# Performance work log

Hardware: AMD Instinct MI355X
Metric: run time of the kernel (lower is better)

Reference implementation:

```python
import jax, jax.numpy as jnp
import numpy as np

N, T, E, H, K = 16, 1024, 1024, 256, 3
MAX_OUT = 4 * T          # static upper bound on upsampled length (padded; torch uses dynamic max)
DUR_FACTOR = 1.0
MIN_DUR = 0
LN_EPS = 1e-5


def setup_inputs() -> dict:
    key = jax.random.key(0)
    ks = jax.random.split(key, 6)
    seqs = jax.random.normal(ks[0], (N, T, E), dtype=jnp.float32)
    lens = jax.random.randint(ks[1], (N,), T // 2, T + 1)
    padding_mask = jnp.arange(T)[None, :] < lens[:, None]  # True = valid frame
    s = 0.02
    return {
        "seqs": seqs,
        "conv1_w": jax.random.normal(ks[2], (H, E, K), jnp.float32) * s,
        "conv1_b": jnp.zeros((H,), jnp.float32),
        "ln1_g": jnp.ones((H,), jnp.float32),
        "ln1_b": jnp.zeros((H,), jnp.float32),
        "conv2_w": jax.random.normal(ks[3], (H, H, K), jnp.float32) * s,
        "conv2_b": jnp.zeros((H,), jnp.float32),
        "ln2_g": jnp.ones((H,), jnp.float32),
        "ln2_b": jnp.zeros((H,), jnp.float32),
        "proj_w": jax.random.normal(ks[4], (H,), jnp.float32) * s,
        "proj_b": jnp.float32(1.1),  # pushes mean duration to ~2 frames
        "padding_mask": padding_mask,
    }


def _conv1d(x, w, b):
    # x: [N, C_in, T], w: [C_out, C_in, K], 'same' padding for K=3
    y = jax.lax.conv_general_dilated(x, w, window_strides=(1,), padding=[(1, 1)],
                                     dimension_numbers=("NCH", "OIH", "NCH"))
    return y + b[None, :, None]


def _layernorm(x, g, b):
    mu = jnp.mean(x, axis=-1, keepdims=True)
    var = jnp.mean(jnp.square(x - mu), axis=-1, keepdims=True)
    return (x - mu) * jax.lax.rsqrt(var + LN_EPS) * g + b


def _variance_predictor(seqs, padding_mask, c1w, c1b, g1, b1, c2w, c2b, g2, b2, pw, pb):
    m = padding_mask[..., None].astype(seqs.dtype)  # [N, T, 1]
    x = seqs * m
    x = jax.nn.relu(_conv1d(x.transpose(0, 2, 1), c1w, c1b)).transpose(0, 2, 1)  # [N, T, H]
    x = _layernorm(x, g1, b1)
    # dropout in eval mode = identity
    x = x * m
    x = jax.nn.relu(_conv1d(x.transpose(0, 2, 1), c2w, c2b)).transpose(0, 2, 1)
    x = _layernorm(x, g2, b2)
    return jnp.einsum("nth,h->nt", x, pw) + pb  # log durations [N, T]


def reference(seqs, conv1_w, conv1_b, ln1_g, ln1_b, conv2_w, conv2_b, ln2_g, ln2_b,
              proj_w, proj_b, padding_mask):
    log_dur = _variance_predictor(seqs, padding_mask, conv1_w, conv1_b, ln1_g, ln1_b,
                                  conv2_w, conv2_b, ln2_g, ln2_b, proj_w, proj_b)
    dur = jnp.round((jnp.exp(log_dur) - 1.0) * DUR_FACTOR).astype(jnp.int32)
    dur = jnp.maximum(dur, MIN_DUR)
    dur = jnp.where(padding_mask, dur, 0)  # apply_padding_mask on integer durations

    # HardUpsampling: output position t takes source frame i = searchsorted(cumsum(dur), t, 'right')
    cum = jnp.cumsum(dur, axis=1)                 # [N, T]
    seq_lens = cum[:, -1]                         # [N]
    pos = jnp.arange(MAX_OUT, dtype=jnp.int32)    # [MAX_OUT]
    idx = jax.vmap(lambda c: jnp.searchsorted(c, pos, side="right"))(cum)  # [N, MAX_OUT]
    idx = jnp.clip(idx, 0, T - 1)
    up = jnp.take_along_axis(seqs, idx[:, :, None], axis=1)  # [N, MAX_OUT, E]
    valid = pos[None, :] < seq_lens[:, None]
    up = jnp.where(valid[:, :, None], up, 0.0)
    return up, seq_lens
```

## Files before the change

### kernel.cpp

```cpp
#include <hip/hip_runtime.h>

#define N_ 16
#define T_ 1024
#define E_ 1024
#define H_ 256
#define MAXOUT 4096
#define M_ (N_ * T_)
#define NJ 768
#define NJ16 48

typedef _Float16 half_t;
typedef __attribute__((ext_vector_type(8))) _Float16 f16x8;
typedef __attribute__((ext_vector_type(4))) _Float16 f16x4;
typedef __attribute__((ext_vector_type(4))) float f32x4;

constexpr size_t Y1_OFF  = 0;
constexpr size_t Y2_OFF  = 25165824;
constexpr size_t A0P_OFF = 50331648;
constexpr size_t A2P_OFF = 83886080;

constexpr size_t B1P_OFF  = 0;
constexpr size_t B2P_OFF  = 1572864;
constexpr size_t DUR_OFF  = 1966080;
constexpr size_t CUM_OFF  = 2031616;

__device__ __forceinline__ float mask_at(const unsigned char* __restrict__ raw, int i) {
    if (raw[1] == 1) return raw[i] ? 1.0f : 0.0f;
    return reinterpret_cast<const int*>(raw)[i] ? 1.0f : 0.0f;
}

__device__ __forceinline__ void gload_lds16(const void* g, void* l) {
    __builtin_amdgcn_global_load_lds(
        (const __attribute__((address_space(1))) unsigned int*)g,
        (__attribute__((address_space(3))) unsigned int*)l, 16, 0, 0);
}

__global__ __launch_bounds__(256) void prep_all_kernel(
    const float* __restrict__ X, const unsigned char* __restrict__ mraw,
    const float* __restrict__ w1, const float* __restrict__ w2,
    half_t* __restrict__ A0p, half_t* __restrict__ B1p, half_t* __restrict__ B2p) {
    const int bid = blockIdx.x;
    if (bid < 1024) {
        const int bm = bid;
        const int l = threadIdx.x & 63;
        const int bk4 = threadIdx.x >> 6;
        const int row = bm * 16 + (l & 15);
        const float mv = mask_at(mraw, row);
        const float* src = X + (size_t)row * E_ + ((l >> 4) * 8);
#pragma unroll
        for (int g = 0; g < 8; ++g) {
            const int bk = g * 4 + bk4;
            float4 v0 = *reinterpret_cast<const float4*>(src + bk * 32);
            float4 v1 = *reinterpret_cast<const float4*>(src + bk * 32 + 4);
            float v[8] = {v0.x, v0.y, v0.z, v0.w, v1.x, v1.y, v1.z, v1.w};
            f16x8 h8;
#pragma unroll
            for (int j = 0; j < 8; ++j) h8[j] = (half_t)(v[j] * mv);
            *reinterpret_cast<f16x8*>(A0p + ((size_t)(bm * 32 + bk) * 64 + l) * 8) = h8;
        }
    } else {
        const bool isW1 = (bid < 1024 + 384);
        const int c = (isW1 ? (bid - 1024) : (bid - 1408)) * 256 + threadIdx.x;
        const int EIN = isW1 ? E_ : H_;
        const float* w = isW1 ? w1 : w2;
        half_t* Bp = isW1 ? B1p : B2p;
        const int l = c & 63;
        const int t = c >> 6;
        const int bj = t % NJ16;
        const int bk = t / NJ16;
        const int j = bj * 16 + (l & 15);
        const int k = j >> 8;
        const int h = j & 255;
        const int e0 = bk * 32 + ((l >> 4) * 8);
        f16x8 h8;
#pragma unroll
        for (int jj = 0; jj < 8; ++jj)
            h8[jj] = (half_t)w[((size_t)h * EIN + e0 + jj) * 3 + k];
        *reinterpret_cast<f16x8*>(Bp + (size_t)c * 8) = h8;
    }
}

template <int NBK>
__global__ __launch_bounds__(256, 4) void gemm_f16_kernel(
    const half_t* __restrict__ Ap, const half_t* __restrict__ Bp,
    half_t* __restrict__ Y) {
    __shared__ __align__(16) half_t lds[2][2][4096];
    const int tid = threadIdx.x;
    const int l = tid & 63;
    const int wv = tid >> 6;
    const int wr = wv >> 1, wc = wv & 1;
    const int bm0 = blockIdx.x * 8;
    const int bj0 = blockIdx.y * 8;

    f32x4 acc[4][4] = {};

    auto stage = [&](int kb, int buf) {
#pragma unroll
        for (int s = 0; s < 2; ++s) {
            const int q = tid + 256 * s;
            const int blk = q >> 6;
            const int ql = q & 63;
            gload_lds16(Ap + (((size_t)(bm0 + blk) * NBK + kb) * 64 + ql) * 8,
                        &lds[buf][0][(size_t)q * 8]);
            gload_lds16(Bp + (((size_t)kb * NJ16 + bj0 + blk) * 64 + ql) * 8,
                        &lds[buf][1][(size_t)q * 8]);
        }
    };

    stage(0, 0);
    int cur = 0;
    for (int kb = 0; kb < NBK; ++kb) {
        __syncthreads();
        if (kb + 1 < NBK) stage(kb + 1, cur ^ 1);

        f16x8 bf[4];
#pragma unroll
        for (int nb = 0; nb < 4; ++nb)
            bf[nb] = *reinterpret_cast<const f16x8*>(&lds[cur][1][((wc * 4 + nb) * 64 + l) * 8]);

        __builtin_amdgcn_s_setprio(1);
#pragma unroll
        for (int mb = 0; mb < 4; ++mb) {
            f16x8 af = *reinterpret_cast<const f16x8*>(&lds[cur][0][((wr * 4 + mb) * 64 + l) * 8]);
#pragma unroll
            for (int nb = 0; nb < 4; ++nb)
                acc[mb][nb] = __builtin_amdgcn_mfma_f32_16x16x32_f16(af, bf[nb], acc[mb][nb], 0, 0, 0);
        }
        __builtin_amdgcn_s_setprio(0);
        cur ^= 1;
    }

    const int mrow0 = blockIdx.x * 128 + wr * 64;
    const int jcol0 = blockIdx.y * 128 + wc * 64;
#pragma unroll
    for (int mb = 0; mb < 4; ++mb)
#pragma unroll
        for (int nb = 0; nb < 4; ++nb) {
            const int j = jcol0 + nb * 16 + (l & 15);
            const int mbase = mrow0 + mb * 16 + (l >> 4) * 4;
#pragma unroll
            for (int r = 0; r < 4; ++r)
                Y[(size_t)(mbase + r) * NJ + j] = (half_t)acc[mb][nb][r];
        }
}

__global__ __launch_bounds__(256) void ln1_kernel(
    const half_t* __restrict__ Y1, const float* __restrict__ cb,
    const float* __restrict__ g, const float* __restrict__ b,
    const unsigned char* __restrict__ mraw,
    half_t* __restrict__ A2p) {
    __shared__ float xs[16][260];
    __shared__ float shs[4], shss[4];
    const int h = threadIdx.x;
    const int bm = blockIdx.x;
    const int wid = h >> 6, lane = h & 63;
    for (int r = 0; r < 16; ++r) {
        const int t = bm * 16 + r;
        float v = (float)Y1[(size_t)t * NJ + 256 + h] + cb[h];
        if ((t & (T_ - 1)) != 0)      v += (float)Y1[(size_t)(t - 1) * NJ + h];
        if ((t & (T_ - 1)) != T_ - 1) v += (float)Y1[(size_t)(t + 1) * NJ + 512 + h];
        v = fmaxf(v, 0.0f);
        float s = v, ss = v * v;
#pragma unroll
        for (int off = 32; off; off >>= 1) {
            s  += __shfl_down(s, off);
            ss += __shfl_down(ss, off);
        }
        if (lane == 0) { shs[wid] = s; shss[wid] = ss; }
        __syncthreads();
        const float S  = shs[0] + shs[1] + shs[2] + shs[3];
        const float SS = shss[0] + shss[1] + shss[2] + shss[3];
        const float mu  = S * (1.0f / H_);
        const float var = SS * (1.0f / H_) - mu * mu;
        const float inv = 1.0f / sqrtf(var + 1e-5f);
        xs[r][h] = ((v - mu) * inv * g[h] + b[h]) * mask_at(mraw, t);
        __syncthreads();
    }
#pragma unroll
    for (int s2 = 0; s2 < 2; ++s2) {
        const int q = threadIdx.x + 256 * s2;
        const int l = q & 63;
        const int bk = q >> 6;
        const int rr = l & 15;
        const int h0 = bk * 32 + ((l >> 4) * 8);
        f16x8 h8;
#pragma unroll
        for (int jj = 0; jj < 8; ++jj) h8[jj] = (half_t)xs[rr][h0 + jj];
        *reinterpret_cast<f16x8*>(A2p + ((size_t)(bm * 8 + bk) * 64 + l) * 8) = h8;
    }
}

__global__ __launch_bounds__(256) void ln2_proj_dur_kernel(
    const half_t* __restrict__ Y2, const float* __restrict__ cb,
    const float* __restrict__ g, const float* __restrict__ b,
    const float* __restrict__ pw, const float* __restrict__ pb,
    const unsigned char* __restrict__ mraw, int* __restrict__ dur) {
    const int t = blockIdx.x * 4 + (threadIdx.x >> 6);
    const int lane = threadIdx.x & 63;
    const int h0 = lane * 4;

    f16x4 c4 = *reinterpret_cast<const f16x4*>(&Y2[(size_t)t * NJ + 256 + h0]);
    float v[4];
#pragma unroll
    for (int i = 0; i < 4; ++i) v[i] = (float)c4[i];
    if ((t & (T_ - 1)) != 0) {
        f16x4 l4 = *reinterpret_cast<const f16x4*>(&Y2[(size_t)(t - 1) * NJ + h0]);
#pragma unroll
        for (int i = 0; i < 4; ++i) v[i] += (float)l4[i];
    }
    if ((t & (T_ - 1)) != T_ - 1) {
        f16x4 r4 = *reinterpret_cast<const f16x4*>(&Y2[(size_t)(t + 1) * NJ + 512 + h0]);
#pragma unroll
        for (int i = 0; i < 4; ++i) v[i] += (float)r4[i];
    }
    float4 cb4 = *reinterpret_cast<const float4*>(&cb[h0]);
    v[0] = fmaxf(v[0] + cb4.x, 0.f); v[1] = fmaxf(v[1] + cb4.y, 0.f);
    v[2] = fmaxf(v[2] + cb4.z, 0.f); v[3] = fmaxf(v[3] + cb4.w, 0.f);

    float s = v[0] + v[1] + v[2] + v[3];
    float ss = v[0]*v[0] + v[1]*v[1] + v[2]*v[2] + v[3]*v[3];
#pragma unroll
    for (int off = 1; off < 64; off <<= 1) {
        s  += __shfl_xor(s, off);
        ss += __shfl_xor(ss, off);
    }
    const float mu  = s * (1.0f / H_);
    const float var = ss * (1.0f / H_) - mu * mu;
    const float inv = 1.0f / sqrtf(var + 1e-5f);

    float4 g4 = *reinterpret_cast<const float4*>(&g[h0]);
    float4 b4 = *reinterpret_cast<const float4*>(&b[h0]);
    float4 p4 = *reinterpret_cast<const float4*>(&pw[h0]);
    float c = ((v[0]-mu)*inv*g4.x + b4.x) * p4.x
            + ((v[1]-mu)*inv*g4.y + b4.y) * p4.y
            + ((v[2]-mu)*inv*g4.z + b4.z) * p4.z
            + ((v[3]-mu)*inv*g4.w + b4.w) * p4.w;
#pragma unroll
    for (int off = 1; off < 64; off <<= 1) c += __shfl_xor(c, off);

    if (lane == 0) {
        const float ld = c + pb[0];
        const float dv = rintf(expf(ld) - 1.0f);
        int di = (int)dv;
        if (di < 0) di = 0;
        if (mask_at(mraw, t) == 0.0f) di = 0;
        dur[t] = di;
    }
}

__global__ __launch_bounds__(1024) void cumsum_kernel(
    const int* __restrict__ dur, int* __restrict__ cum,
    float* __restrict__ seq_lens_out) {
    __shared__ int s[1024];
    const int n = blockIdx.x, t = threadIdx.x;
    s[t] = dur[n * T_ + t];
    __syncthreads();
    for (int off = 1; off < 1024; off <<= 1) {
        int v = (t >= off) ? s[t - off] : 0;
        __syncthreads();
        s[t] += v;
        __syncthreads();
    }
    cum[n * T_ + t] = s[t];
    if (t == T_ - 1) seq_lens_out[n] = (float)s[t];
}

__global__ __launch_bounds__(256) void upsample_kernel(
    const float* __restrict__ seqs, const int* __restrict__ cum,
    float* __restrict__ out) {
    const int wid = blockIdx.x * 4 + (threadIdx.x >> 6);
    const int n = wid >> 12;
    const int p = wid & (MAXOUT - 1);
    const int lane = threadIdx.x & 63;
    const int* c = cum + n * T_;
    const int slen = c[T_ - 1];
    int lo = 0, hi = T_;
    while (lo < hi) {
        int mid = (lo + hi) >> 1;
        if (c[mid] <= p) lo = mid + 1; else hi = mid;
    }
    const int idx = (lo < T_ - 1) ? lo : (T_ - 1);
    const bool valid = (p < slen);
    const f32x4* src = reinterpret_cast<const f32x4*>(seqs + ((size_t)(n * T_ + idx) * E_));
    f32x4* dst = reinterpret_cast<f32x4*>(out + (size_t)wid * E_);
#pragma unroll
    for (int i = 0; i < 4; ++i) {
        f32x4 v = {0.f, 0.f, 0.f, 0.f};
        if (valid) v = src[lane + 64 * i];
        __builtin_nontemporal_store(v, &dst[lane + 64 * i]);
    }
}

extern "C" void kernel_launch(void* const* d_in, const int* in_sizes, int n_in,
                              void* d_out, int out_size, void* d_ws, size_t ws_size,
                              hipStream_t stream) {
    const float* seqs = (const float*)d_in[0];
    const float* w1   = (const float*)d_in[1];
    const float* b1   = (const float*)d_in[2];
    const float* g1   = (const float*)d_in[3];
    const float* bb1  = (const float*)d_in[4];
    const float* w2   = (const float*)d_in[5];
    const float* b2   = (const float*)d_in[6];
    const float* g2   = (const float*)d_in[7];
    const float* bb2  = (const float*)d_in[8];
    const float* pw   = (const float*)d_in[9];
    const float* pb   = (const float*)d_in[10];
    const unsigned char* mraw = (const unsigned char*)d_in[11];

    char* wsb = (char*)d_ws;
    half_t* B1p = (half_t*)(wsb + B1P_OFF);
    half_t* B2p = (half_t*)(wsb + B2P_OFF);
    int* dur = (int*)(wsb + DUR_OFF);
    int* cum = (int*)(wsb + CUM_OFF);

    char* outb = (char*)d_out;
    half_t* Y1  = (half_t*)(outb + Y1_OFF);
    half_t* Y2  = (half_t*)(outb + Y2_OFF);
    half_t* A0p = (half_t*)(outb + A0P_OFF);
    half_t* A2p = (half_t*)(outb + A2P_OFF);

    float* out      = (float*)d_out;
    float* slen_out = out + (size_t)N_ * MAXOUT * E_;

    prep_all_kernel<<<1504, 256, 0, stream>>>(seqs, mraw, w1, w2, A0p, B1p, B2p);
    gemm_f16_kernel<32><<<dim3(M_ / 128, NJ / 128), 256, 0, stream>>>(A0p, B1p, Y1);
    ln1_kernel<<<M_ / 16, 256, 0, stream>>>(Y1, b1, g1, bb1, mraw, A2p);
    gemm_f16_kernel<8><<<dim3(M_ / 128, NJ / 128), 256, 0, stream>>>(A2p, B2p, Y2);
    ln2_proj_dur_kernel<<<M_ / 4, 256, 0, stream>>>(Y2, b2, g2, bb2, pw, pb, mraw, dur);
    cumsum_kernel<<<N_, 1024, 0, stream>>>(dur, cum, slen_out);
    upsample_kernel<<<(N_ * MAXOUT) / 4, 256, 0, stream>>>(seqs, cum, out);
}
```

Before: 152.1 us.

## Fuse fp32 input masking and fp16 conversion into first conv GEMM A-load

Removes the separate pass that masked seqs, converted it to fp16 and packed it into A0p. The first GEMM now reads fp32 rows directly, applies the mask, converts in registers and writes to LDS. B fragments are loaded straight from global memory into registers with double buffering instead of going through LDS. The grid is reordered so blocks sharing an A tile run adjacently, and the launch bound drops to 2 blocks per SM. This saves a 32MB fp16 write and reread, at the cost of reading twice as many A bytes (fp32) inside the GEMM, higher register pressure and lower occupancy.

```diff
diff --git a/kernel.cpp b/kernel.cpp
--- a/kernel.cpp
+++ b/kernel.cpp
@@ -16,8 +16,7 @@
 
 constexpr size_t Y1_OFF  = 0;
 constexpr size_t Y2_OFF  = 25165824;
-constexpr size_t A0P_OFF = 50331648;
-constexpr size_t A2P_OFF = 83886080;
+constexpr size_t A2P_OFF = 50331648;
 
 constexpr size_t B1P_OFF  = 0;
 constexpr size_t B2P_OFF  = 1572864;
@@ -35,103 +34,132 @@
         (__attribute__((address_space(3))) unsigned int*)l, 16, 0, 0);
 }
 
-__global__ __launch_bounds__(256) void prep_all_kernel(
-    const float* __restrict__ X, const unsigned char* __restrict__ mraw,
+__global__ __launch_bounds__(256) void prep_w_kernel(
     const float* __restrict__ w1, const float* __restrict__ w2,
-    half_t* __restrict__ A0p, half_t* __restrict__ B1p, half_t* __restrict__ B2p) {
+    half_t* __restrict__ B1p, half_t* __restrict__ B2p) {
     const int bid = blockIdx.x;
-    if (bid < 1024) {
-        const int bm = bid;
-        const int l = threadIdx.x & 63;
-        const int bk4 = threadIdx.x >> 6;
-        const int row = bm * 16 + (l & 15);
-        const float mv = mask_at(mraw, row);
-        const float* src = X + (size_t)row * E_ + ((l >> 4) * 8);
-#pragma unroll
-        for (int g = 0; g < 8; ++g) {
-            const int bk = g * 4 + bk4;
-            float4 v0 = *reinterpret_cast<const float4*>(src + bk * 32);
-            float4 v1 = *reinterpret_cast<const float4*>(src + bk * 32 + 4);
-            float v[8] = {v0.x, v0.y, v0.z, v0.w, v1.x, v1.y, v1.z, v1.w};
-            f16x8 h8;
-#pragma unroll
-            for (int j = 0; j < 8; ++j) h8[j] = (half_t)(v[j] * mv);
-            *reinterpret_cast<f16x8*>(A0p + ((size_t)(bm * 32 + bk) * 64 + l) * 8) = h8;
-        }
-    } else {
-        const bool isW1 = (bid < 1024 + 384);
-        const int c = (isW1 ? (bid - 1024) : (bid - 1408)) * 256 + threadIdx.x;
-        const int EIN = isW1 ? E_ : H_;
-        const float* w = isW1 ? w1 : w2;
-        half_t* Bp = isW1 ? B1p : B2p;
-        const int l = c & 63;
-        const int t = c >> 6;
-        const int bj = t % NJ16;
-        const int bk = t / NJ16;
-        const int j = bj * 16 + (l & 15);
-        const int k = j >> 8;
-        const int h = j & 255;
-        const int e0 = bk * 32 + ((l >> 4) * 8);
-        f16x8 h8;
-#pragma unroll
-        for (int jj = 0; jj < 8; ++jj)
-            h8[jj] = (half_t)w[((size_t)h * EIN + e0 + jj) * 3 + k];
-        *reinterpret_cast<f16x8*>(Bp + (size_t)c * 8) = h8;
-    }
-}
-
-template <int NBK>
-__global__ __launch_bounds__(256, 4) void gemm_f16_kernel(
-    const half_t* __restrict__ Ap, const half_t* __restrict__ Bp,
-    half_t* __restrict__ Y) {
-    __shared__ __align__(16) half_t lds[2][2][4096];
+    const bool isW1 = (bid < 384);
+    const int c = (isW1 ? bid : bid - 384) * 256 + threadIdx.x;
+    const int EIN = isW1 ? E_ : H_;
+    const float* w = isW1 ? w1 : w2;
+    half_t* Bp = isW1 ? B1p : B2p;
+    const int l = c & 63;
+    const int t = c >> 6;
+    const int bj = t % NJ16;
+    const int bk = t / NJ16;
+    const int j = bj * 16 + (l & 15);
+    const int k = j >> 8;
+    const int h = j & 255;
+    const int e0 = bk * 32 + ((l >> 4) * 8);
+    f16x8 h8;
+#pragma unroll
+    for (int jj = 0; jj < 8; ++jj)
+        h8[jj] = (half_t)w[((size_t)h * EIN + e0 + jj) * 3 + k];
+    *reinterpret_cast<f16x8*>(Bp + (size_t)c * 8) = h8;
+}
+
+template <int NBK, bool AF32>
+__global__ __launch_bounds__(256, 2) void gemm_kernel(
+    const float* __restrict__ Af32, const half_t* __restrict__ Af16,
+    const unsigned char* __restrict__ mraw,
+    const half_t* __restrict__ Bp, half_t* __restrict__ Y) {
+    __shared__ __align__(16) half_t lds[2][4096];
     const int tid = threadIdx.x;
     const int l = tid & 63;
     const int wv = tid >> 6;
     const int wr = wv >> 1, wc = wv & 1;
-    const int bm0 = blockIdx.x * 8;
-    const int bj0 = blockIdx.y * 8;
+    const int bj0 = blockIdx.x * 8;
+    const int bm0 = blockIdx.y * 8;
 
     f32x4 acc[4][4] = {};
-
-    auto stage = [&](int kb, int buf) {
-#pragma unroll
-        for (int s = 0; s < 2; ++s) {
-            const int q = tid + 256 * s;
-            const int blk = q >> 6;
-            const int ql = q & 63;
-            gload_lds16(Ap + (((size_t)(bm0 + blk) * NBK + kb) * 64 + ql) * 8,
-                        &lds[buf][0][(size_t)q * 8]);
-            gload_lds16(Bp + (((size_t)kb * NJ16 + bj0 + blk) * 64 + ql) * 8,
-                        &lds[buf][1][(size_t)q * 8]);
-        }
+    f16x8 bA[4], bB[4];
+    f32x4 rA[4];
+
+    const int blk = tid >> 6;
+    const int m1 = bm0 * 16 + blk * 16 + (l & 15);
+    const int m2 = m1 + 64;
+    const int cbase = (l >> 4) * 8;
+
+    const float *pA1 = nullptr, *pA2 = nullptr;
+    const half_t *qA1 = nullptr, *qA2 = nullptr;
+    float mv1 = 0.f, mv2 = 0.f;
+    if constexpr (AF32) {
+        mv1 = mask_at(mraw, m1);
+        mv2 = mask_at(mraw, m2);
+        pA1 = Af32 + (size_t)m1 * (NBK * 32) + cbase;
+        pA2 = Af32 + (size_t)m2 * (NBK * 32) + cbase;
+    } else {
+        qA1 = Af16 + (size_t)(bm0 + blk) * NBK * 512 + l * 8;
+        qA2 = Af16 + (size_t)(bm0 + blk + 4) * NBK * 512 + l * 8;
+    }
+    const half_t* pB = Bp + ((size_t)(bj0 + wc * 4) * 64 + l) * 8;
+
+    auto loadB = [&](int kb, f16x8 (&dst)[4]) {
+#pragma unroll
+        for (int nb = 0; nb < 4; ++nb)
+            dst[nb] = *reinterpret_cast<const f16x8*>(
+                pB + (size_t)kb * (NJ16 * 512) + nb * 512);
     };
-
-    stage(0, 0);
-    int cur = 0;
-    for (int kb = 0; kb < NBK; ++kb) {
-        __syncthreads();
-        if (kb + 1 < NBK) stage(kb + 1, cur ^ 1);
-
-        f16x8 bf[4];
-#pragma unroll
-        for (int nb = 0; nb < 4; ++nb)
-            bf[nb] = *reinterpret_cast<const f16x8*>(&lds[cur][1][((wc * 4 + nb) * 64 + l) * 8]);
-
+    auto issueA = [&](int kb, int buf) {
+        if constexpr (AF32) {
+            rA[0] = *reinterpret_cast<const f32x4*>(pA1 + kb * 32);
+            rA[1] = *reinterpret_cast<const f32x4*>(pA1 + kb * 32 + 4);
+            rA[2] = *reinterpret_cast<const f32x4*>(pA2 + kb * 32);
+            rA[3] = *reinterpret_cast<const f32x4*>(pA2 + kb * 32 + 4);
+        } else {
+            gload_lds16(qA1 + (size_t)kb * 512, &lds[buf][(size_t)tid * 8]);
+            gload_lds16(qA2 + (size_t)kb * 512, &lds[buf][(size_t)(tid + 256) * 8]);
+        }
+    };
+    auto writeA = [&](int buf) {
+        f16x8 h1, h2;
+#pragma unroll
+        for (int j = 0; j < 4; ++j) {
+            h1[j]     = (half_t)(rA[0][j] * mv1);
+            h1[4 + j] = (half_t)(rA[1][j] * mv1);
+            h2[j]     = (half_t)(rA[2][j] * mv2);
+            h2[4 + j] = (half_t)(rA[3][j] * mv2);
+        }
+        *reinterpret_cast<f16x8*>(&lds[buf][(size_t)tid * 8]) = h1;
+        *reinterpret_cast<f16x8*>(&lds[buf][(size_t)(tid + 256) * 8]) = h2;
+    };
+
+    issueA(0, 0);
+    if constexpr (AF32) writeA(0);
+    loadB(0, bA);
+    __syncthreads();
+
+    auto body = [&](int kb, int cur, f16x8 (&bc)[4], f16x8 (&bn)[4]) {
+        if (kb + 1 < NBK) {
+            issueA(kb + 1, cur ^ 1);
+            loadB(kb + 1, bn);
+        }
+        f16x8 af[4];
+#pragma unroll
+        for (int mb = 0; mb < 4; ++mb)
+            af[mb] = *reinterpret_cast<const f16x8*>(
+                &lds[cur][((wr * 4 + mb) * 64 + l) * 8]);
         __builtin_amdgcn_s_setprio(1);
 #pragma unroll
-        for (int mb = 0; mb < 4; ++mb) {
-            f16x8 af = *reinterpret_cast<const f16x8*>(&lds[cur][0][((wr * 4 + mb) * 64 + l) * 8]);
+        for (int mb = 0; mb < 4; ++mb)
 #pragma unroll
             for (int nb = 0; nb < 4; ++nb)
-                acc[mb][nb] = __builtin_amdgcn_mfma_f32_16x16x32_f16(af, bf[nb], acc[mb][nb], 0, 0, 0);
-        }
+                acc[mb][nb] = __builtin_amdgcn_mfma_f32_16x16x32_f16(
+                    af[mb], bc[nb], acc[mb][nb], 0, 0, 0);
         __builtin_amdgcn_s_setprio(0);
-        cur ^= 1;
-    }
-
-    const int mrow0 = blockIdx.x * 128 + wr * 64;
-    const int jcol0 = blockIdx.y * 128 + wc * 64;
+        if constexpr (AF32) {
+            if (kb + 1 < NBK) writeA(cur ^ 1);
+        }
+        __syncthreads();
+    };
+
+    for (int kb = 0; kb < NBK; kb += 2) {
+        body(kb, 0, bA, bB);
+        body(kb + 1, 1, bB, bA);
+    }
+
+    const int jcol0 = blockIdx.x * 128 + wc * 64;
+    const int mrow0 = blockIdx.y * 128 + wr * 64;
 #pragma unroll
     for (int mb = 0; mb < 4; ++mb)
 #pragma unroll
@@ -316,16 +344,17 @@
     char* outb = (char*)d_out;
     half_t* Y1  = (half_t*)(outb + Y1_OFF);
     half_t* Y2  = (half_t*)(outb + Y2_OFF);
-    half_t* A0p = (half_t*)(outb + A0P_OFF);
     half_t* A2p = (half_t*)(outb + A2P_OFF);
 
     float* out      = (float*)d_out;
     float* slen_out = out + (size_t)N_ * MAXOUT * E_;
 
-    prep_all_kernel<<<1504, 256, 0, stream>>>(seqs, mraw, w1, w2, A0p, B1p, B2p);
-    gemm_f16_kernel<32><<<dim3(M_ / 128, NJ / 128), 256, 0, stream>>>(A0p, B1p, Y1);
+    prep_w_kernel<<<480, 256, 0, stream>>>(w1, w2, B1p, B2p);
+    gemm_kernel<32, true><<<dim3(NJ / 128, M_ / 128), 256, 0, stream>>>(
+        seqs, nullptr, mraw, B1p, Y1);
     ln1_kernel<<<M_ / 16, 256, 0, stream>>>(Y1, b1, g1, bb1, mraw, A2p);
-    gemm_f16_kernel<8><<<dim3(M_ / 128, NJ / 128), 256, 0, stream>>>(A2p, B2p, Y2);
+    gemm_kernel<8, false><<<dim3(NJ / 128, M_ / 128), 256, 0, stream>>>(
+        nullptr, A2p, mraw, B2p, Y2);
     ln2_proj_dur_kernel<<<M_ / 4, 256, 0, stream>>>(Y2, b2, g2, bb2, pw, pb, mraw, dur);
     cumsum_kernel<<<N_, 1024, 0, stream>>>(dur, cum, slen_out);
     upsample_kernel<<<(N_ * MAXOUT) / 4, 256, 0, stream>>>(seqs, cum, out);
```

New measurement: 175.1 us. 1.15x slower.

## Remap GEMM blocks XCD-aware and vectorize LN1 with one wave per row

Applied to the files above, without the earlier changes.

The GEMM launches change from a 2D grid to a 1D grid of 768 blocks. Each block's index is remapped so that consecutive blocks dispatched round-robin across the 8 XCDs share nearby M rows and all 6 column tiles. This should improve L2 reuse of the A and B tiles per XCD. LN1 is also rewritten so each wave handles four rows with 4-wide vectorized loads and a wave-level xor-shuffle reduction, which removes the per-row block barriers and shared-memory reduction.

```diff
diff --git a/kernel.cpp b/kernel.cpp
--- a/kernel.cpp
+++ b/kernel.cpp
@@ -89,8 +89,13 @@
     const int l = tid & 63;
     const int wv = tid >> 6;
     const int wr = wv >> 1, wc = wv & 1;
-    const int bm0 = blockIdx.x * 8;
-    const int bj0 = blockIdx.y * 8;
+
+    const int d = blockIdx.x;
+    const int work = (d & 7) * 96 + (d >> 3);
+    const int bjIdx = work % 6;
+    const int bmIdx = work / 6;
+    const int bm0 = bmIdx * 8;
+    const int bj0 = bjIdx * 8;
 
     f32x4 acc[4][4] = {};
 
@@ -130,8 +135,8 @@
         cur ^= 1;
     }
 
-    const int mrow0 = blockIdx.x * 128 + wr * 64;
-    const int jcol0 = blockIdx.y * 128 + wc * 64;
+    const int mrow0 = bmIdx * 128 + wr * 64;
+    const int jcol0 = bjIdx * 128 + wc * 64;
 #pragma unroll
     for (int mb = 0; mb < 4; ++mb)
 #pragma unroll
@@ -150,42 +155,62 @@
     const unsigned char* __restrict__ mraw,
     half_t* __restrict__ A2p) {
     __shared__ float xs[16][260];
-    __shared__ float shs[4], shss[4];
-    const int h = threadIdx.x;
     const int bm = blockIdx.x;
-    const int wid = h >> 6, lane = h & 63;
-    for (int r = 0; r < 16; ++r) {
+    const int wvv = threadIdx.x >> 6;
+    const int lane = threadIdx.x & 63;
+    const int h0 = lane * 4;
+    const float4 cb4 = *reinterpret_cast<const float4*>(&cb[h0]);
+    const float4 g4  = *reinterpret_cast<const float4*>(&g[h0]);
+    const float4 b4  = *reinterpret_cast<const float4*>(&b[h0]);
+#pragma unroll
+    for (int i = 0; i < 4; ++i) {
+        const int r = wvv * 4 + i;
         const int t = bm * 16 + r;
-        float v = (float)Y1[(size_t)t * NJ + 256 + h] + cb[h];
-        if ((t & (T_ - 1)) != 0)      v += (float)Y1[(size_t)(t - 1) * NJ + h];
-        if ((t & (T_ - 1)) != T_ - 1) v += (float)Y1[(size_t)(t + 1) * NJ + 512 + h];
-        v = fmaxf(v, 0.0f);
-        float s = v, ss = v * v;
-#pragma unroll
-        for (int off = 32; off; off >>= 1) {
-            s  += __shfl_down(s, off);
-            ss += __shfl_down(ss, off);
-        }
-        if (lane == 0) { shs[wid] = s; shss[wid] = ss; }
-        __syncthreads();
-        const float S  = shs[0] + shs[1] + shs[2] + shs[3];
-        const float SS = shss[0] + shss[1] + shss[2] + shss[3];
-        const float mu  = S * (1.0f / H_);
-        const float var = SS * (1.0f / H_) - mu * mu;
+        f16x4 c4 = *reinterpret_cast<const f16x4*>(&Y1[(size_t)t * NJ + 256 + h0]);
+        float v[4];
+#pragma unroll
+        for (int j = 0; j < 4; ++j) v[j] = (float)c4[j];
+        if ((t & (T_ - 1)) != 0) {
+            f16x4 l4 = *reinterpret_cast<const f16x4*>(&Y1[(size_t)(t - 1) * NJ + h0]);
+#pragma unroll
+            for (int j = 0; j < 4; ++j) v[j] += (float)l4[j];
+        }
+        if ((t & (T_ - 1)) != T_ - 1) {
+            f16x4 r4 = *reinterpret_cast<const f16x4*>(&Y1[(size_t)(t + 1) * NJ + 512 + h0]);
+#pragma unroll
+            for (int j = 0; j < 4; ++j) v[j] += (float)r4[j];
+        }
+        v[0] = fmaxf(v[0] + cb4.x, 0.f); v[1] = fmaxf(v[1] + cb4.y, 0.f);
+        v[2] = fmaxf(v[2] + cb4.z, 0.f); v[3] = fmaxf(v[3] + cb4.w, 0.f);
+        float s  = v[0] + v[1] + v[2] + v[3];
+        float ss = v[0]*v[0] + v[1]*v[1] + v[2]*v[2] + v[3]*v[3];
+#pragma unroll
+        for (int off = 1; off < 64; off <<= 1) {
+            s  += __shfl_xor(s, off);
+            ss += __shfl_xor(ss, off);
+        }
+        const float mu  = s * (1.0f / H_);
+        const float var = ss * (1.0f / H_) - mu * mu;
         const float inv = 1.0f / sqrtf(var + 1e-5f);
-        xs[r][h] = ((v - mu) * inv * g[h] + b[h]) * mask_at(mraw, t);
-        __syncthreads();
-    }
+        const float mv = mask_at(mraw, t);
+        float4 o;
+        o.x = ((v[0] - mu) * inv * g4.x + b4.x) * mv;
+        o.y = ((v[1] - mu) * inv * g4.y + b4.y) * mv;
+        o.z = ((v[2] - mu) * inv * g4.z + b4.z) * mv;
+        o.w = ((v[3] - mu) * inv * g4.w + b4.w) * mv;
+        *reinterpret_cast<float4*>(&xs[r][h0]) = o;
+    }
+    __syncthreads();
 #pragma unroll
     for (int s2 = 0; s2 < 2; ++s2) {
         const int q = threadIdx.x + 256 * s2;
         const int l = q & 63;
         const int bk = q >> 6;
         const int rr = l & 15;
-        const int h0 = bk * 32 + ((l >> 4) * 8);
+        const int hh = bk * 32 + ((l >> 4) * 8);
         f16x8 h8;
 #pragma unroll
-        for (int jj = 0; jj < 8; ++jj) h8[jj] = (half_t)xs[rr][h0 + jj];
+        for (int jj = 0; jj < 8; ++jj) h8[jj] = (half_t)xs[rr][hh + jj];
         *reinterpret_cast<f16x8*>(A2p + ((size_t)(bm * 8 + bk) * 64 + l) * 8) = h8;
     }
 }
@@ -323,9 +348,9 @@
     float* slen_out = out + (size_t)N_ * MAXOUT * E_;
 
     prep_all_kernel<<<1504, 256, 0, stream>>>(seqs, mraw, w1, w2, A0p, B1p, B2p);
-    gemm_f16_kernel<32><<<dim3(M_ / 128, NJ / 128), 256, 0, stream>>>(A0p, B1p, Y1);
+    gemm_f16_kernel<32><<<768, 256, 0, stream>>>(A0p, B1p, Y1);
     ln1_kernel<<<M_ / 16, 256, 0, stream>>>(Y1, b1, g1, bb1, mraw, A2p);
-    gemm_f16_kernel<8><<<dim3(M_ / 128, NJ / 128), 256, 0, stream>>>(A2p, B2p, Y2);
+    gemm_f16_kernel<8><<<768, 256, 0, stream>>>(A2p, B2p, Y2);
     ln2_proj_dur_kernel<<<M_ / 4, 256, 0, stream>>>(Y2, b2, g2, bb2, pw, pb, mraw, dur);
     cumsum_kernel<<<N_, 1024, 0, stream>>>(dur, cum, slen_out);
     upsample_kernel<<<(N_ * MAXOUT) / 4, 256, 0, stream>>>(seqs, cum, out);
```

Result: faster. 134.7 us (-11.4%).
